# Optimization experiments

Hardware: AMD Instinct MI355X
Metric: run time of the kernel (lower is better)

## Reference

```python
import jax, jax.numpy as jnp
import numpy as np

H = 256
NUM_REL = 460
NUM_ENT = 20000
B = 4096
CUR_TS = 10
PATH_LEN = 8


def _gru_step(x, h, W_ih, W_hh, b_ih, b_hh):
    # PyTorch GRUCell math
    gi = x @ W_ih.T + b_ih          # [B, 3H]
    gh = h @ W_hh.T + b_hh          # [B, 3H]
    ir, iz, inn = jnp.split(gi, 3, axis=1)
    hr, hz, hn = jnp.split(gh, 3, axis=1)
    r = jax.nn.sigmoid(ir + hr)
    z = jax.nn.sigmoid(iz + hz)
    n = jnp.tanh(inn + r * hn)
    return (1.0 - z) * n + z * h


def setup_inputs() -> dict:
    key = jax.random.key(0)
    ks = jax.random.split(key, 24)
    s = 1.0 / np.sqrt(H)
    f32 = jnp.float32
    d = {
        "pre_emb": jax.random.normal(ks[0], (NUM_ENT, H), f32),
        "r_emb": jax.random.normal(ks[1], (NUM_REL, H), f32),
        "partial_embeding": jax.random.normal(ks[2], (B, CUR_TS * NUM_REL), f32),
        # params (uniform-ish linear init scaled by 1/sqrt(H))
        "W_map1": jax.random.normal(ks[3], (2 * H, H), f32) * s,
        "b_map1": jax.random.normal(ks[4], (2 * H,), f32) * s,
        "W_map2": jax.random.normal(ks[5], (H, 2 * H), f32) * s,
        "b_map2": jax.random.normal(ks[6], (H,), f32) * s,
        "W_h1": jax.random.normal(ks[7], (H, H), f32) * s,
        "b_h1": jax.random.normal(ks[8], (H,), f32) * s,
        "W_h2": jax.random.normal(ks[9], (H, H), f32) * s,
        "b_h2": jax.random.normal(ks[10], (H,), f32) * s,
        "W_attn": jax.random.normal(ks[11], (H, H), f32) * s,
        "b_attn": jax.random.normal(ks[12], (H,), f32) * s,
        "W_align": jax.random.normal(ks[13], (H, H), f32) * s,
        "b_align": jax.random.normal(ks[14], (H,), f32) * s,
        "W_ih": jax.random.normal(ks[15], (3 * H, H), f32) * s,
        "W_hh": jax.random.normal(ks[16], (3 * H, H), f32) * s,
        "b_ih": jax.random.normal(ks[17], (3 * H,), f32) * s,
        "b_hh": jax.random.normal(ks[18], (3 * H,), f32) * s,
        "all_triples": jax.random.randint(ks[19], (B, 3), 0, NUM_REL, dtype=jnp.int64)
        if jax.config.jax_enable_x64 else jax.random.randint(ks[19], (B, 3), 0, NUM_REL, dtype=jnp.int32),
        "cur_ts": CUR_TS,
        "num_rel": NUM_REL,
    }
    return d


def reference(pre_emb, r_emb, partial_embeding,
              W_map1, b_map1, W_map2, b_map2,
              W_h1, b_h1, W_h2, b_h2,
              W_attn, b_attn, W_align, b_align,
              W_ih, W_hh, b_ih, b_hh,
              all_triples, cur_ts, num_rel):
    # rel_mapping1 -> rel_mapping2
    mapped_rel = (r_emb @ W_map1.T + b_map1) @ W_map2.T + b_map2     # [R, H]
    q_rel = mapped_rel[all_triples[:, 1]]                            # [B, H]

    # attention logits base (constant over timesteps): linear_attn(q_rel) @ mapped_rel.T
    attn_base = (q_rel @ W_attn.T + b_attn) @ mapped_rel.T           # [B, R]

    start_ts = max(cur_ts - PATH_LEN, 0)
    nb = partial_embeding.shape[0]
    cur_seq = partial_embeding.reshape(nb, cur_ts, num_rel)[:, start_ts:cur_ts]  # [B, T, R]
    cur_seq = jnp.swapaxes(cur_seq, 0, 1)                            # [T, B, R]

    h0 = jnp.zeros((nb, H), dtype=pre_emb.dtype)

    def step(h, cur):
        attn = cur * attn_base
        attn = jnp.where(attn == 0, jnp.asarray(-1e9, attn.dtype), attn)
        attn = jax.nn.softmax(attn, axis=1)
        x = attn @ mapped_rel                                        # [B, H]
        return _gru_step(x, h, W_ih, W_hh, b_ih, b_hh), None

    gru_hidden, _ = jax.lax.scan(step, h0, cur_seq)

    # predicted history embedding + match loss (MSE)
    predicted_hist = 0.1 * ((q_rel @ W_h1.T + b_h1) @ W_h2.T + b_h2) + q_rel
    match_loss = jnp.mean((predicted_hist - gru_hidden) ** 2)

    # forward_forth, distmult scoring
    h2 = _gru_step(q_rel, predicted_hist, W_ih, W_hh, b_ih, b_hh)    # [B, H]
    aligned_all = pre_emb @ W_align.T + b_align                      # [E, H]
    sub = aligned_all[all_triples[:, 0]]                             # [B, H]
    score_logits = (sub * h2) @ aligned_all.T                        # [B, E]
    score = jax.nn.sigmoid(score_logits)

    # BCE(sigmoid(logits), one_hot(obj)) in stable logits form without
    # materializing the dense one-hot label matrix:
    # mean over B*E of [ softplus(x) - x * label ]
    obj = all_triples[:, 2]
    pos_logits = score_logits[jnp.arange(nb), obj]
    path_loss = (jnp.sum(jax.nn.softplus(score_logits)) - jnp.sum(pos_logits)) / (nb * score_logits.shape[1])

    return match_loss, path_loss, score
```

## Files before the change

### kernel.cpp

```cpp
#include <hip/hip_runtime.h>
#include <hip/hip_bf16.h>

typedef __hip_bfloat16 bf16;
typedef __attribute__((ext_vector_type(8))) short short8;
typedef __attribute__((ext_vector_type(4))) float f32x4;
typedef __attribute__((ext_vector_type(4))) short short4v;

#define NREL 460
#define KP   480
#define NENT 20000
#define NENT_PAD 20224
#define NB   4096

__device__ inline float sigmoidf_(float x){ return 1.f/(1.f+__expf(-x)); }

__device__ inline void gload16(const bf16* g, bf16* l){
  __builtin_amdgcn_global_load_lds(
      (const __attribute__((address_space(1))) unsigned int*)g,
      (__attribute__((address_space(3))) unsigned int*)l, 16, 0, 0);
}

__device__ __forceinline__ void fgemm_body(
    const float* __restrict__ A, int lda, int arows,
    const float* __restrict__ B, int ldb,
    const float* __restrict__ bias,
    float* __restrict__ C, int ldc, int K, int mode,
    const float* __restrict__ add_src, bf16* __restrict__ ct_out,
    float* As, float* Bs, int bx, int by)
{
  const int tid = threadIdx.x;
  const int row0 = bx*64, col0 = by*64;
  const int tx = tid & 15, ty = tid >> 4;
  float acc[4][4] = {};
  for (int k0 = 0; k0 < K; k0 += 32){
    __syncthreads();
    #pragma unroll
    for (int s = 0; s < 2; ++s){
      int slot = tid + s*256;
      int r = slot >> 3, c4 = (slot & 7)*4;
      int ra = row0 + r; if (ra >= arows) ra = arows - 1;
      float4 v = *(const float4*)(A + (long)ra*lda + k0 + c4);
      As[(c4+0)*68+r] = v.x; As[(c4+1)*68+r] = v.y; As[(c4+2)*68+r] = v.z; As[(c4+3)*68+r] = v.w;
      float4 w = *(const float4*)(B + (long)(col0 + r)*ldb + k0 + c4);
      Bs[(c4+0)*68+r] = w.x; Bs[(c4+1)*68+r] = w.y; Bs[(c4+2)*68+r] = w.z; Bs[(c4+3)*68+r] = w.w;
    }
    __syncthreads();
    #pragma unroll
    for (int kk = 0; kk < 32; ++kk){
      float4 a4 = *(const float4*)(&As[kk*68 + ty*4]);
      float4 b4 = *(const float4*)(&Bs[kk*68 + tx*4]);
      float av[4] = {a4.x, a4.y, a4.z, a4.w};
      float bv[4] = {b4.x, b4.y, b4.z, b4.w};
      #pragma unroll
      for (int i = 0; i < 4; ++i)
        #pragma unroll
        for (int j = 0; j < 4; ++j) acc[i][j] += av[i]*bv[j];
    }
  }
  const int rb = row0 + ty*4, cb = col0 + tx*4;
  if (mode == 1){
    #pragma unroll
    for (int i = 0; i < 4; ++i){
      float4 v = {acc[i][0], acc[i][1], acc[i][2], acc[i][3]};
      *(float4*)(C + (long)(rb+i)*ldc + cb) = v;
      int rr = rb + i;
      if (rr < KP){
        #pragma unroll
        for (int j = 0; j < 4; ++j)
          ct_out[(cb+j)*KP + rr] = __float2bfloat16(rr < NREL ? acc[i][j] : 0.f);
      }
    }
  } else if (mode == 2){
    #pragma unroll
    for (int i = 0; i < 4; ++i){
      float4 v;
      #pragma unroll
      for (int j = 0; j < 4; ++j)
        ((float*)&v)[j] = 0.1f*(acc[i][j] + bias[cb+j]) + add_src[(long)(rb+i)*ldc + cb+j];
      *(float4*)(C + (long)(rb+i)*ldc + cb) = v;
    }
  } else {
    float bv[4] = {0,0,0,0};
    if (bias){ bv[0]=bias[cb]; bv[1]=bias[cb+1]; bv[2]=bias[cb+2]; bv[3]=bias[cb+3]; }
    #pragma unroll
    for (int i = 0; i < 4; ++i){
      float4 v = {acc[i][0]+bv[0], acc[i][1]+bv[1], acc[i][2]+bv[2], acc[i][3]+bv[3]};
      *(float4*)(C + (long)(rb+i)*ldc + cb) = v;
    }
  }
}

struct FDesc {
  const float* A; const float* B; const float* bias; float* C;
  const float* add; bf16* ct;
  int lda, ldb, ldc, K, arows, mode;
};

template<int MODE>
__device__ __forceinline__ void gemm128_body(
    const bf16* __restrict__ A, int lda,
    const bf16* __restrict__ B, int ldb,
    const float* __restrict__ bias,
    void* __restrict__ C, long ldc,
    int K, int n_valid, double* __restrict__ sp_sum,
    const int* __restrict__ trips,
    bf16* sbuf, float* wsum, int bx, int by)
{
  const int tid = threadIdx.x;
  const int lane = tid & 63, wave = tid >> 6;
  const long row0 = (long)bx * 128;
  const long col0 = (long)by * 128;
  const int sr = tid >> 2;
  const int sc = ((tid & 3) ^ ((sr >> 1) & 3)) * 8;
  const bf16* Ag0 = A + (row0 + sr)*lda + sc;
  const bf16* Ag1 = A + (row0 + 64 + sr)*lda + sc;
  const bf16* Bg0 = B + (col0 + sr)*ldb + sc;
  const bf16* Bg1 = B + (col0 + 64 + sr)*ldb + sc;
  bf16* As_ = sbuf;
  bf16* Bs_ = sbuf + 8192;
  const int wr = (wave >> 1)*64, wc = (wave & 1)*64;
  const int rA = lane & 15;
  const int kA = ((lane >> 4) ^ ((rA >> 1) & 3)) * 8;
  f32x4 acc[4][4] = {};
  const int nt = K >> 5;
  gload16(Ag0, As_ + tid*8);
  gload16(Ag1, As_ + 2048 + tid*8);
  gload16(Bg0, Bs_ + tid*8);
  gload16(Bg1, Bs_ + 2048 + tid*8);
  int cur = 0;
  for (int t = 0; t < nt; ++t){
    if (t + 1 < nt){
      const int k0 = (t+1) << 5;
      const int nxt = cur ^ 1;
      gload16(Ag0 + k0, As_ + nxt*4096 + tid*8);
      gload16(Ag1 + k0, As_ + nxt*4096 + 2048 + tid*8);
      gload16(Bg0 + k0, Bs_ + nxt*4096 + tid*8);
      gload16(Bg1 + k0, Bs_ + nxt*4096 + 2048 + tid*8);
      asm volatile("s_waitcnt vmcnt(4)" ::: "memory");
    } else {
      asm volatile("s_waitcnt vmcnt(0)" ::: "memory");
    }
    __builtin_amdgcn_s_barrier();
    short8 a[4], b[4];
    #pragma unroll
    for (int m = 0; m < 4; ++m) a[m] = *(const short8*)(As_ + cur*4096 + (wr + m*16 + rA)*32 + kA);
    #pragma unroll
    for (int n = 0; n < 4; ++n) b[n] = *(const short8*)(Bs_ + cur*4096 + (wc + n*16 + rA)*32 + kA);
    asm volatile("s_waitcnt lgkmcnt(0)" ::: "memory");
    __builtin_amdgcn_s_barrier();
    #pragma unroll
    for (int m = 0; m < 4; ++m)
      #pragma unroll
      for (int n = 0; n < 4; ++n)
        acc[m][n] = __builtin_amdgcn_mfma_f32_16x16x32_bf16(a[m], b[n], acc[m][n], 0,0,0);
    cur ^= 1;
  }
  const int ri = (lane >> 4)*4, ci = lane & 15;
  __syncthreads();
  if constexpr (MODE == 1){
    bf16* epi = sbuf + wave*1152;
    const int rrow = lane >> 2, q = lane & 3;
    #pragma unroll
    for (int m = 0; m < 4; ++m){
      #pragma unroll
      for (int n = 0; n < 4; ++n){
        long c = col0 + wc + n*16 + ci;
        float bv = bias ? bias[c] : 0.f;
        #pragma unroll
        for (int i = 0; i < 4; ++i)
          epi[(ri+i)*72 + n*16 + ci] = __float2bfloat16(acc[m][n][i] + bv);
      }
      long gr = row0 + wr + m*16 + rrow;
      bf16* gp = (bf16*)C + gr*ldc + col0 + wc + q*16;
      const bf16* lp = epi + rrow*72 + q*16;
      *(short8*)(gp)     = *(const short8*)(lp);
      *(short8*)(gp + 8) = *(const short8*)(lp + 8);
    }
  } else {
    float* epi = (float*)sbuf + wave*1088;
    const int rrow = lane >> 2, q = lane & 3;
    const bool maybe = (col0 + wc) < 464;
    float spart = 0.f, ppart = 0.f;
    #pragma unroll
    for (int m = 0; m < 4; ++m){
      int obj[4];
      if (maybe){
        #pragma unroll
        for (int i = 0; i < 4; ++i)
          obj[i] = trips[3*(int)(row0 + wr + m*16 + ri + i) + 2];
      }
      #pragma unroll
      for (int n = 0; n < 4; ++n){
        long c = col0 + wc + n*16 + ci;
        bool cv = (c < n_valid);
        #pragma unroll
        for (int i = 0; i < 4; ++i){
          float v = acc[m][n][i];
          float sg = 0.f;
          if (cv){
            float e = __expf(-fabsf(v));
            float tt = 1.f + e;
            float rr = __builtin_amdgcn_rcpf(tt);
            sg = (v >= 0.f) ? rr : 1.f - rr;
            spart += fmaxf(v, 0.f) + e*(0.9404f - 0.2537f*e);
            if (maybe && c == obj[i]) ppart += v;
          }
          epi[(ri+i)*68 + n*16 + ci + 2] = sg;
        }
      }
      long gr = row0 + wr + m*16 + rrow;
      long c16 = col0 + wc + q*16;
      if (c16 < n_valid){
        float* gp = (float*)C + gr*ldc + c16;
        const float* lp = epi + rrow*68 + q*16 + 2;
        *(float2*)(gp)      = *(const float2*)(lp);
        *(float4*)(gp + 2)  = *(const float4*)(lp + 2);
        *(float4*)(gp + 6)  = *(const float4*)(lp + 6);
        *(float4*)(gp + 10) = *(const float4*)(lp + 10);
        *(float2*)(gp + 14) = *(const float2*)(lp + 14);
      }
    }
    #pragma unroll
    for (int off = 32; off >= 1; off >>= 1){
      spart += __shfl_xor(spart, off);
      ppart += __shfl_xor(ppart, off);
    }
    if (lane == 0){ wsum[wave] = spart; wsum[4+wave] = ppart; }
    __syncthreads();
    if (tid == 0)
      atomicAdd(sp_sum, (double)(wsum[0]+wsum[1]+wsum[2]+wsum[3]));
    if (tid == 1)
      atomicAdd(sp_sum+1, (double)(wsum[4]+wsum[5]+wsum[6]+wsum[7]));
  }
}

__global__ __launch_bounds__(256) void k_conv_g1(
    const float4* __restrict__ s0, short4v* __restrict__ d0, int n0,
    const float4* __restrict__ s1, short4v* __restrict__ d1, int n1,
    const float4* __restrict__ s2, short4v* __restrict__ d2, int n2,
    short4v* __restrict__ pad0, int n3, double* __restrict__ dz,
    const float* __restrict__ gA, const float* __restrict__ gB,
    const float* __restrict__ gbias, float* __restrict__ gC)
{
  __shared__ __align__(16) float As[32*68];
  __shared__ __align__(16) float Bs[32*68];
  int bid = blockIdx.x;
  if (bid < 64){
    fgemm_body(gA,256,NREL, gB,256, gbias, gC,512, 256, 0, nullptr,nullptr,
               As, Bs, bid&7, bid>>3);
    return;
  }
  int i = (bid-64)*256 + threadIdx.x;
  if (i < n0+n1+n2){
    const float4* s; short4v* d; int j;
    if (i < n0){ s = s0; d = d0; j = i; }
    else if (i < n0+n1){ s = s1; d = d1; j = i-n0; }
    else { s = s2; d = d2; j = i-n0-n1; }
    float4 v = s[j];
    bf16 a = __float2bfloat16(v.x), b = __float2bfloat16(v.y);
    bf16 c = __float2bfloat16(v.z), e = __float2bfloat16(v.w);
    short4v o; o.x = *(short*)&a; o.y = *(short*)&b; o.z = *(short*)&c; o.w = *(short*)&e;
    d[j] = o;
  } else if (i < n0+n1+n2+n3){
    short4v z = {0,0,0,0};
    pad0[i - (n0+n1+n2)] = z;
  } else if (i < n0+n1+n2+n3+8){
    dz[i - (n0+n1+n2+n3)] = 0.0;
  }
}

__global__ __launch_bounds__(256) void k_fgemm(
    const float* A, int lda, int arows, const float* B, int ldb,
    const float* bias, float* C, int ldc, int K, int mode,
    const float* add_src, bf16* ct_out){
  __shared__ __align__(16) float As[32*68];
  __shared__ __align__(16) float Bs[32*68];
  fgemm_body(A, lda, arows, B, ldb, bias, C, ldc, K, mode, add_src, ct_out,
             As, Bs, blockIdx.x, blockIdx.y);
}

__global__ __launch_bounds__(256) void k_fgemm_multi(FDesc d0, FDesc d1, FDesc d2,
                                                     int y1, int y2){
  __shared__ __align__(16) float As[32*68];
  __shared__ __align__(16) float Bs[32*68];
  int y = blockIdx.y;
  FDesc d; int by;
  if (y < y1){ d = d0; by = y; }
  else if (y < y2){ d = d1; by = y - y1; }
  else { d = d2; by = y - y2; }
  fgemm_body(d.A, d.lda, d.arows, d.B, d.ldb, d.bias, d.C, d.ldc, d.K, d.mode,
             d.add, d.ct, As, Bs, blockIdx.x, by);
}

__global__ __launch_bounds__(256) void k_g3_aligned(
    FDesc d0, FDesc d1, FDesc d2, int y1, int y2,
    const bf16* __restrict__ pA, const bf16* __restrict__ pB,
    const float* __restrict__ pbias, bf16* __restrict__ pC)
{
  __shared__ __align__(16) char smem[34816 + 32];
  int bid = blockIdx.x;
  if (bid < 160){
    int bx = bid & 7, y = bid >> 3;
    FDesc d; int by;
    if (y < y1){ d = d0; by = y; }
    else if (y < y2){ d = d1; by = y - y1; }
    else { d = d2; by = y - y2; }
    fgemm_body(d.A, d.lda, d.arows, d.B, d.ldb, d.bias, d.C, d.ldc, d.K, d.mode,
               d.add, d.ct, (float*)smem, (float*)(smem + 17408), bx, by);
  } else {
    int idx = bid - 160;
    gemm128_body<1>(pA, 256, pB, 256, pbias, pC, 256, 256, 0, nullptr, nullptr,
                    (bf16*)smem, (float*)(smem + 34816), idx % 158, idx / 158);
  }
}

__global__ __launch_bounds__(256) void k_soft_makep(const float* __restrict__ partial,
    const float* __restrict__ attn_base, const int* __restrict__ trips,
    bf16* __restrict__ attn_all,
    const bf16* __restrict__ Qbf,
    const float* __restrict__ M_ih, const float* __restrict__ ghp,
    const float* __restrict__ ph, const float* __restrict__ b_ih,
    bf16* __restrict__ P){
  int bid = blockIdx.x;
  if (bid >= NB/4){
    int i = (bid - NB/4)*256 + threadIdx.x;
    int b = i >> 8, k = i & 255;
    int s = trips[b*3+0], rel = trips[b*3+1];
    long rb = (long)rel*768;
    float rg = sigmoidf_(M_ih[rb+k]     + b_ih[k]     + ghp[rb+k]);
    float zg = sigmoidf_(M_ih[rb+256+k] + b_ih[256+k] + ghp[rb+256+k]);
    float ng = tanhf    (M_ih[rb+512+k] + b_ih[512+k] + rg*ghp[rb+512+k]);
    float h2v = (1.f - zg)*ng + zg*ph[rel*256+k];
    P[i] = __float2bfloat16(__bfloat162float(Qbf[(long)s*256+k]) * h2v);
    return;
  }
  int wave = threadIdx.x >> 6, lane = threadIdx.x & 63;
  int b = bid*4 + wave;
  int rel = trips[b*3+1];
  const float* base = attn_base + (long)rel*512;
  float bs[8];
  #pragma unroll
  for (int s = 0; s < 8; ++s){
    int idx = s*64 + lane;
    bs[s] = (idx < NREL) ? base[idx] : 0.f;
  }
  const float* cur0 = partial + (long)b*4600 + 2*NREL;
  for (int t = 0; t < 8; ++t){
    const float* cur = cur0 + t*NREL;
    float v[8]; float mx = -1e30f;
    #pragma unroll
    for (int s = 0; s < 8; ++s){
      int idx = s*64 + lane;
      float val = -1e30f;
      if (idx < NREL){
        float pz = cur[idx]*bs[s];
        val = (pz == 0.f) ? -1e9f : pz;
      }
      v[s] = val; mx = fmaxf(mx, val);
    }
    #pragma unroll
    for (int off = 32; off >= 1; off >>= 1) mx = fmaxf(mx, __shfl_xor(mx, off));
    float sum = 0.f;
    #pragma unroll
    for (int s = 0; s < 8; ++s){
      int idx = s*64 + lane;
      if (idx < NREL){ v[s] = __expf(v[s]-mx); sum += v[s]; }
    }
    #pragma unroll
    for (int off = 32; off >= 1; off >>= 1) sum += __shfl_xor(sum, off);
    float inv = 1.f/sum;
    long obase = ((long)t*NB + b)*KP;
    #pragma unroll
    for (int s = 0; s < 8; ++s){
      int idx = s*64 + lane;
      if (idx < KP) attn_all[obase + idx] = __float2bfloat16(idx < NREL ? v[s]*inv : 0.f);
    }
  }
}

__global__ __launch_bounds__(256) void k_gemm_dual(
    const bf16* __restrict__ A2, const bf16* __restrict__ B2,
    void* __restrict__ C2, long ldc2, int K2, int nvalid2,
    double* __restrict__ sp, const int* __restrict__ trips, int nblk2,
    const bf16* __restrict__ A1, const bf16* __restrict__ B1,
    const float* __restrict__ bias1, void* __restrict__ C1, long ldc1, int K1)
{
  __shared__ __align__(16) bf16 sbuf[16384];
  __shared__ float wsum[8];
  int bid = blockIdx.x;
  if (bid < nblk2){
    gemm128_body<2>(A2, 256, B2, 256, nullptr, C2, ldc2, K2, nvalid2, sp, trips,
                    sbuf, wsum, bid & 31, bid >> 5);
  } else {
    int idx = bid - nblk2;
    gemm128_body<1>(A1, KP, B1, KP, bias1, C1, ldc1, K1, 0, nullptr, nullptr,
                    sbuf, wsum, idx & 255, idx >> 8);
  }
}

__global__ __launch_bounds__(512) void k_scan(
    const bf16* __restrict__ gi_all,
    const bf16* __restrict__ W_hh_bf,
    const float* __restrict__ b_hh,
    const float* __restrict__ ph,
    const int* __restrict__ trips,
    double* __restrict__ dsum, int* __restrict__ done, float* __restrict__ outf)
{
  __shared__ __align__(16) bf16 hl[16*264];
  __shared__ __align__(16) bf16 gbuf[2][16*768];
  __shared__ float red[8];
  const int tid = threadIdx.x;
  const int lane = tid & 63, wave = tid >> 6;
  const int brow0 = blockIdx.x * 16;
  const int rA = lane & 15, kA = (lane >> 4) * 8;
  const int ci = lane & 15, rbase = (lane >> 4) * 4;
  float hreg[2][4] = {};
  float bh[3][2];
  #pragma unroll
  for (int f = 0; f < 2; ++f){
    int cf = wave*32 + f*16 + ci;
    bh[0][f] = b_hh[cf]; bh[1][f] = b_hh[256+cf]; bh[2][f] = b_hh[512+cf];
  }
  short8 warr[3][2][6];
  #pragma unroll
  for (int g = 0; g < 3; ++g)
    #pragma unroll
    for (int f = 0; f < 2; ++f)
      #pragma unroll
      for (int k = 0; k < 6; ++k)
        warr[g][f][k] = *(const short8*)(W_hh_bf + (g*256 + wave*32 + f*16 + rA)*256 + k*32 + kA);
  {
    const bf16* src = gi_all + (long)brow0 * 768;
    #pragma unroll
    for (int i = 0; i < 3; ++i){
      int off = (wave*3 + i)*512 + lane*8;
      gload16(src + off, gbuf[0] + off);
    }
  }
  int cur = 0;
  for (int t = 0; t < 8; ++t){
    f32x4 acc[3][2] = {};
    if (t > 0){
      #pragma unroll
      for (int k = 0; k < 8; ++k){
        short8 a = *(const short8*)(hl + rA*264 + k*32 + kA);
        #pragma unroll
        for (int g = 0; g < 3; ++g)
          #pragma unroll
          for (int f = 0; f < 2; ++f){
            short8 b;
            if (k < 6) b = warr[g][f][k];
            else b = *(const short8*)(W_hh_bf + (g*256 + wave*32 + f*16 + rA)*256 + k*32 + kA);
            acc[g][f] = __builtin_amdgcn_mfma_f32_16x16x32_bf16(a, b, acc[g][f], 0,0,0);
          }
      }
    }
    asm volatile("s_waitcnt lgkmcnt(0) vmcnt(0)" ::: "memory");
    __builtin_amdgcn_s_barrier();
    if (t < 7){
      const bf16* src = gi_all + ((long)(t+1)*NB + brow0) * 768;
      bf16* dst = gbuf[cur ^ 1];
      #pragma unroll
      for (int i = 0; i < 3; ++i){
        int off = (wave*3 + i)*512 + lane*8;
        gload16(src + off, dst + off);
      }
    }
    const bf16* gl = gbuf[cur];
    #pragma unroll
    for (int f = 0; f < 2; ++f){
      int cf = wave*32 + f*16 + ci;
      #pragma unroll
      for (int i = 0; i < 4; ++i){
        int rloc = rbase + i;
        float gir = __bfloat162float(gl[rloc*768 + cf]);
        float giz = __bfloat162float(gl[rloc*768 + 256 + cf]);
        float gin = __bfloat162float(gl[rloc*768 + 512 + cf]);
        float rg = sigmoidf_(gir + acc[0][f][i] + bh[0][f]);
        float zg = sigmoidf_(giz + acc[1][f][i] + bh[1][f]);
        float ng = tanhf(gin + rg*(acc[2][f][i] + bh[2][f]));
        float hn = (1.f - zg)*ng + zg*hreg[f][i];
        hreg[f][i] = hn;
        hl[rloc*264 + cf] = __float2bfloat16(hn);
      }
    }
    asm volatile("s_waitcnt lgkmcnt(0)" ::: "memory");
    __builtin_amdgcn_s_barrier();
    cur ^= 1;
  }
  float d = 0.f;
  #pragma unroll
  for (int f = 0; f < 2; ++f){
    int cf = wave*32 + f*16 + ci;
    #pragma unroll
    for (int i = 0; i < 4; ++i){
      int rel = trips[(brow0 + rbase + i)*3 + 1];
      float diff = ph[rel*256 + cf] - hreg[f][i];
      d += diff*diff;
    }
  }
  #pragma unroll
  for (int off = 32; off >= 1; off >>= 1) d += __shfl_xor(d, off);
  if (lane == 0) red[wave] = d;
  __syncthreads();
  if (tid == 0){
    float s = 0.f;
    #pragma unroll
    for (int w = 0; w < 8; ++w) s += red[w];
    atomicAdd(dsum, (double)s);
    asm volatile("s_waitcnt vmcnt(0)" ::: "memory");
    int ticket = atomicAdd(done, 1);
    if (ticket == (int)gridDim.x - 1){
      double m  = atomicAdd(dsum+0, 0.0);
      double sp = atomicAdd(dsum+1, 0.0);
      double pp = atomicAdd(dsum+2, 0.0);
      outf[0] = (float)(m / (4096.0*256.0));
      outf[1] = (float)((sp - pp) / (4096.0*20000.0));
    }
  }
}

extern "C" void kernel_launch(void* const* d_in, const int* in_sizes, int n_in,
                              void* d_out, int out_size, void* d_ws, size_t ws_size,
                              hipStream_t stream){
  const float* pre_emb = (const float*)d_in[0];
  const float* r_emb   = (const float*)d_in[1];
  const float* partial = (const float*)d_in[2];
  const float* W_map1  = (const float*)d_in[3];
  const float* b_map1  = (const float*)d_in[4];
  const float* W_map2  = (const float*)d_in[5];
  const float* b_map2  = (const float*)d_in[6];
  const float* W_h1    = (const float*)d_in[7];
  const float* b_h1    = (const float*)d_in[8];
  const float* W_h2    = (const float*)d_in[9];
  const float* b_h2    = (const float*)d_in[10];
  const float* W_attn  = (const float*)d_in[11];
  const float* b_attn  = (const float*)d_in[12];
  const float* W_align = (const float*)d_in[13];
  const float* b_align = (const float*)d_in[14];
  const float* W_ih    = (const float*)d_in[15];
  const float* W_hh    = (const float*)d_in[16];
  const float* b_ih    = (const float*)d_in[17];
  const float* b_hh    = (const float*)d_in[18];
  const int*   trips   = (const int*)d_in[19];
  float* out = (float*)d_out;

  char* w = (char*)d_ws;
  auto alloc = [&](size_t bytes)->char*{
    char* r = w; w += (bytes + 255) & ~size_t(255); return r;
  };
  double* dsum      = (double*)alloc(128);
  int*    done      = (int*)(dsum + 4);
  float* t1         = (float*)alloc(512*512*4);
  float* mapped     = (float*)alloc(512*256*4);
  float* a1         = (float*)alloc(512*256*4);
  float* th         = (float*)alloc(512*256*4);
  float* ph         = (float*)alloc(512*256*4);
  float* M_ih       = (float*)alloc(512*768*4);
  float* ghp        = (float*)alloc(512*768*4);
  float* attn_base  = (float*)alloc(512*512*4);
  bf16*  M_ihT      = (bf16*)alloc(768*KP*2);
  bf16*  W_hh_bf    = (bf16*)alloc(768*256*2);
  bf16*  W_align_bf = (bf16*)alloc(256*256*2);
  bf16*  Q_bf       = (bf16*)alloc((size_t)NENT_PAD*256*2);
  bf16*  P_bf       = (bf16*)alloc((size_t)NB*256*2);
  bf16*  attn_all   = (bf16*)alloc((size_t)8*NB*KP*2);
  bf16*  gi_all     = (bf16*)alloc((size_t)8*NB*768*2);
  bf16*  pre_bf     = attn_all;

  {
    int n0 = NENT*256/4, n1 = 768*256/4, n2 = 256*256/4;
    int n3 = (NENT_PAD-NENT)*256/4;
    int ntot = n0+n1+n2+n3+8;
    k_conv_g1<<<64 + (ntot+255)/256, 256, 0, stream>>>(
        (const float4*)pre_emb, (short4v*)pre_bf, n0,
        (const float4*)W_hh, (short4v*)W_hh_bf, n1,
        (const float4*)W_align, (short4v*)W_align_bf, n2,
        (short4v*)(pre_bf + (size_t)NENT*256), n3, dsum,
        r_emb, W_map1, b_map1, t1);
  }
  k_fgemm<<<dim3(8,4),256,0,stream>>>(t1,512,512, W_map2,512, b_map2, mapped,256, 512, 0, nullptr, nullptr);
  {
    FDesc d0 = { mapped, W_ih,   nullptr, M_ih, nullptr, M_ihT, 256, 256, 768, 256, 512, 1 };
    FDesc d1 = { mapped, W_attn, b_attn,  a1,   nullptr, nullptr, 256, 256, 256, 256, 512, 0 };
    FDesc d2 = { mapped, W_h1,   b_h1,    th,   nullptr, nullptr, 256, 256, 256, 256, 512, 0 };
    k_g3_aligned<<<160 + 316, 256, 0, stream>>>(d0, d1, d2, 12, 16,
                                                pre_bf, W_align_bf, b_align, Q_bf);
  }
  {
    FDesc d0 = { th, W_h2,   b_h2,    ph,        mapped,  nullptr, 256, 256, 256, 256, 512, 2 };
    FDesc d1 = { a1, mapped, nullptr, attn_base, nullptr, nullptr, 256, 256, 512, 256, 512, 0 };
    k_fgemm_multi<<<dim3(8,12),256,0,stream>>>(d0, d1, d1, 4, 12);
  }
  k_fgemm<<<dim3(8,12),256,0,stream>>>(ph,256,512, W_hh,256, b_hh, ghp,768, 256, 0, nullptr, nullptr);
  k_soft_makep<<<NB/4 + NB,256,0,stream>>>(partial, attn_base, trips, attn_all,
                                           Q_bf, M_ih, ghp, ph, b_ih, P_bf);
  k_gemm_dual<<<5056 + 1536, 256, 0, stream>>>(
      P_bf, Q_bf, out+2, NENT, 256, NENT, dsum+1, trips, 5056,
      attn_all, M_ihT, b_ih, gi_all, 768, KP);
  k_scan<<<NB/16,512,0,stream>>>(gi_all, W_hh_bf, b_hh, ph, trips, dsum, done, out);
}
```

Measured before the change: 386.9 us.

## Run dual GEMM with 512-thread blocks splitting 128x128 tile over eight waves

```diff
diff --git a/kernel.cpp b/kernel.cpp
--- a/kernel.cpp
+++ b/kernel.cpp
@@ -96,15 +96,12 @@
   int lda, ldb, ldc, K, arows, mode;
 };
 
-template<int MODE>
-__device__ __forceinline__ void gemm128_body(
+__device__ __forceinline__ void gemm128_body1(
     const bf16* __restrict__ A, int lda,
     const bf16* __restrict__ B, int ldb,
     const float* __restrict__ bias,
-    void* __restrict__ C, long ldc,
-    int K, int n_valid, double* __restrict__ sp_sum,
-    const int* __restrict__ trips,
-    bf16* sbuf, float* wsum, int bx, int by)
+    bf16* __restrict__ C, long ldc, int K,
+    bf16* sbuf, int bx, int by)
 {
   const int tid = threadIdx.x;
   const int lane = tid & 63, wave = tid >> 6;
@@ -157,28 +154,101 @@
   }
   const int ri = (lane >> 4)*4, ci = lane & 15;
   __syncthreads();
+  bf16* epi = sbuf + wave*1152;
+  const int rrow = lane >> 2, q = lane & 3;
+  #pragma unroll
+  for (int m = 0; m < 4; ++m){
+    #pragma unroll
+    for (int n = 0; n < 4; ++n){
+      long c = col0 + wc + n*16 + ci;
+      float bv = bias ? bias[c] : 0.f;
+      #pragma unroll
+      for (int i = 0; i < 4; ++i)
+        epi[(ri+i)*72 + n*16 + ci] = __float2bfloat16(acc[m][n][i] + bv);
+    }
+    long gr = row0 + wr + m*16 + rrow;
+    bf16* gp = C + gr*ldc + col0 + wc + q*16;
+    const bf16* lp = epi + rrow*72 + q*16;
+    *(short8*)(gp)     = *(const short8*)(lp);
+    *(short8*)(gp + 8) = *(const short8*)(lp + 8);
+  }
+}
+
+template<int MODE>
+__device__ __forceinline__ void gemm512_body(
+    const bf16* __restrict__ A, int lda,
+    const bf16* __restrict__ B, int ldb,
+    const float* __restrict__ bias,
+    void* __restrict__ C, long ldc,
+    int K, int n_valid, double* __restrict__ sp_sum,
+    const int* __restrict__ trips,
+    bf16* sbuf, float* wsum, int bx, int by)
+{
+  const int tid = threadIdx.x;
+  const int lane = tid & 63, wave = tid >> 6;
+  const long row0 = (long)bx * 128;
+  const long col0 = (long)by * 128;
+  const int sr = tid >> 2;
+  const int sc = ((tid & 3) ^ ((sr >> 1) & 3)) * 8;
+  const bf16* Ag = A + (row0 + sr)*lda + sc;
+  const bf16* Bg = B + (col0 + sr)*ldb + sc;
+  bf16* As_ = sbuf;
+  bf16* Bs_ = sbuf + 8192;
+  const int wr = (wave >> 2)*64, wc = (wave & 3)*32;
+  const int rA = lane & 15;
+  const int kA = ((lane >> 4) ^ ((rA >> 1) & 3)) * 8;
+  f32x4 acc[4][2] = {};
+  const int nt = K >> 5;
+  gload16(Ag, As_ + tid*8);
+  gload16(Bg, Bs_ + tid*8);
+  int cur = 0;
+  for (int t = 0; t < nt; ++t){
+    if (t + 1 < nt){
+      const int k0 = (t+1) << 5;
+      const int nxt = cur ^ 1;
+      gload16(Ag + k0, As_ + nxt*4096 + tid*8);
+      gload16(Bg + k0, Bs_ + nxt*4096 + tid*8);
+      asm volatile("s_waitcnt vmcnt(2)" ::: "memory");
+    } else {
+      asm volatile("s_waitcnt vmcnt(0)" ::: "memory");
+    }
+    __builtin_amdgcn_s_barrier();
+    short8 a[4], b[2];
+    #pragma unroll
+    for (int m = 0; m < 4; ++m) a[m] = *(const short8*)(As_ + cur*4096 + (wr + m*16 + rA)*32 + kA);
+    #pragma unroll
+    for (int n = 0; n < 2; ++n) b[n] = *(const short8*)(Bs_ + cur*4096 + (wc + n*16 + rA)*32 + kA);
+    asm volatile("s_waitcnt lgkmcnt(0)" ::: "memory");
+    __builtin_amdgcn_s_barrier();
+    #pragma unroll
+    for (int m = 0; m < 4; ++m)
+      #pragma unroll
+      for (int n = 0; n < 2; ++n)
+        acc[m][n] = __builtin_amdgcn_mfma_f32_16x16x32_bf16(a[m], b[n], acc[m][n], 0,0,0);
+    cur ^= 1;
+  }
+  const int ri = (lane >> 4)*4, ci = lane & 15;
+  __syncthreads();
   if constexpr (MODE == 1){
-    bf16* epi = sbuf + wave*1152;
-    const int rrow = lane >> 2, q = lane & 3;
+    bf16* epi = sbuf + wave*640;
+    const int rw = lane >> 2, q = lane & 3;
     #pragma unroll
     for (int m = 0; m < 4; ++m){
       #pragma unroll
-      for (int n = 0; n < 4; ++n){
+      for (int n = 0; n < 2; ++n){
         long c = col0 + wc + n*16 + ci;
         float bv = bias ? bias[c] : 0.f;
         #pragma unroll
         for (int i = 0; i < 4; ++i)
-          epi[(ri+i)*72 + n*16 + ci] = __float2bfloat16(acc[m][n][i] + bv);
-      }
-      long gr = row0 + wr + m*16 + rrow;
-      bf16* gp = (bf16*)C + gr*ldc + col0 + wc + q*16;
-      const bf16* lp = epi + rrow*72 + q*16;
-      *(short8*)(gp)     = *(const short8*)(lp);
-      *(short8*)(gp + 8) = *(const short8*)(lp + 8);
+          epi[(ri+i)*40 + n*16 + ci] = __float2bfloat16(acc[m][n][i] + bv);
+      }
+      long gr = row0 + wr + m*16 + rw;
+      bf16* gp = (bf16*)C + gr*ldc + col0 + wc + q*8;
+      *(short8*)(gp) = *(const short8*)(epi + rw*40 + q*8);
     }
   } else {
-    float* epi = (float*)sbuf + wave*1088;
-    const int rrow = lane >> 2, q = lane & 3;
+    float* epi = (float*)sbuf + wave*576;
+    const int rw = lane >> 2, q = lane & 3;
     const bool maybe = (col0 + wc) < 464;
     float spart = 0.f, ppart = 0.f;
     #pragma unroll
@@ -190,7 +260,7 @@
           obj[i] = trips[3*(int)(row0 + wr + m*16 + ri + i) + 2];
       }
       #pragma unroll
-      for (int n = 0; n < 4; ++n){
+      for (int n = 0; n < 2; ++n){
         long c = col0 + wc + n*16 + ci;
         bool cv = (c < n_valid);
         #pragma unroll
@@ -205,19 +275,17 @@
             spart += fmaxf(v, 0.f) + e*(0.9404f - 0.2537f*e);
             if (maybe && c == obj[i]) ppart += v;
           }
-          epi[(ri+i)*68 + n*16 + ci + 2] = sg;
+          epi[(ri+i)*36 + n*16 + ci + 2] = sg;
         }
       }
-      long gr = row0 + wr + m*16 + rrow;
-      long c16 = col0 + wc + q*16;
-      if (c16 < n_valid){
-        float* gp = (float*)C + gr*ldc + c16;
-        const float* lp = epi + rrow*68 + q*16 + 2;
-        *(float2*)(gp)      = *(const float2*)(lp);
-        *(float4*)(gp + 2)  = *(const float4*)(lp + 2);
-        *(float4*)(gp + 6)  = *(const float4*)(lp + 6);
-        *(float4*)(gp + 10) = *(const float4*)(lp + 10);
-        *(float2*)(gp + 14) = *(const float2*)(lp + 14);
+      long gr = row0 + wr + m*16 + rw;
+      long c8 = col0 + wc + q*8;
+      if (c8 < n_valid){
+        float* gp = (float*)C + gr*ldc + c8;
+        const float* lp = epi + rw*36 + q*8 + 2;
+        *(float2*)(gp)     = *(const float2*)(lp);
+        *(float4*)(gp + 2) = *(const float4*)(lp + 2);
+        *(float2*)(gp + 6) = *(const float2*)(lp + 6);
       }
     }
     #pragma unroll
@@ -225,12 +293,20 @@
       spart += __shfl_xor(spart, off);
       ppart += __shfl_xor(ppart, off);
     }
-    if (lane == 0){ wsum[wave] = spart; wsum[4+wave] = ppart; }
+    if (lane == 0){ wsum[wave] = spart; wsum[8+wave] = ppart; }
     __syncthreads();
-    if (tid == 0)
-      atomicAdd(sp_sum, (double)(wsum[0]+wsum[1]+wsum[2]+wsum[3]));
-    if (tid == 1)
-      atomicAdd(sp_sum+1, (double)(wsum[4]+wsum[5]+wsum[6]+wsum[7]));
+    if (tid == 0){
+      float s = 0.f;
+      #pragma unroll
+      for (int w = 0; w < 8; ++w) s += wsum[w];
+      atomicAdd(sp_sum, (double)s);
+    }
+    if (tid == 1){
+      float p = 0.f;
+      #pragma unroll
+      for (int w = 0; w < 8; ++w) p += wsum[8+w];
+      atomicAdd(sp_sum+1, (double)p);
+    }
   }
 }
 
@@ -297,7 +373,7 @@
     const bf16* __restrict__ pA, const bf16* __restrict__ pB,
     const float* __restrict__ pbias, bf16* __restrict__ pC)
 {
-  __shared__ __align__(16) char smem[34816 + 32];
+  __shared__ __align__(16) char smem[34816];
   int bid = blockIdx.x;
   if (bid < 160){
     int bx = bid & 7, y = bid >> 3;
@@ -309,8 +385,8 @@
                d.add, d.ct, (float*)smem, (float*)(smem + 17408), bx, by);
   } else {
     int idx = bid - 160;
-    gemm128_body<1>(pA, 256, pB, 256, pbias, pC, 256, 256, 0, nullptr, nullptr,
-                    (bf16*)smem, (float*)(smem + 34816), idx % 158, idx / 158);
+    gemm128_body1(pA, 256, pB, 256, pbias, pC, 256, 256,
+                  (bf16*)smem, idx % 158, idx / 158);
   }
 }
 
@@ -378,7 +454,7 @@
   }
 }
 
-__global__ __launch_bounds__(256) void k_gemm_dual(
+__global__ __launch_bounds__(512, 4) void k_gemm_dual(
     const bf16* __restrict__ A2, const bf16* __restrict__ B2,
     void* __restrict__ C2, long ldc2, int K2, int nvalid2,
     double* __restrict__ sp, const int* __restrict__ trips, int nblk2,
@@ -386,14 +462,14 @@
     const float* __restrict__ bias1, void* __restrict__ C1, long ldc1, int K1)
 {
   __shared__ __align__(16) bf16 sbuf[16384];
-  __shared__ float wsum[8];
+  __shared__ float wsum[16];
   int bid = blockIdx.x;
   if (bid < nblk2){
-    gemm128_body<2>(A2, 256, B2, 256, nullptr, C2, ldc2, K2, nvalid2, sp, trips,
+    gemm512_body<2>(A2, 256, B2, 256, nullptr, C2, ldc2, K2, nvalid2, sp, trips,
                     sbuf, wsum, bid & 31, bid >> 5);
   } else {
     int idx = bid - nblk2;
-    gemm128_body<1>(A1, KP, B1, KP, bias1, C1, ldc1, K1, 0, nullptr, nullptr,
+    gemm512_body<1>(A1, KP, B1, KP, bias1, C1, ldc1, K1, 0, nullptr, nullptr,
                     sbuf, wsum, idx & 255, idx >> 8);
   }
 }
@@ -595,7 +671,7 @@
   k_fgemm<<<dim3(8,12),256,0,stream>>>(ph,256,512, W_hh,256, b_hh, ghp,768, 256, 0, nullptr, nullptr);
   k_soft_makep<<<NB/4 + NB,256,0,stream>>>(partial, attn_base, trips, attn_all,
                                            Q_bf, M_ih, ghp, ph, b_ih, P_bf);
-  k_gemm_dual<<<5056 + 1536, 256, 0, stream>>>(
+  k_gemm_dual<<<5056 + 1536, 512, 0, stream>>>(
       P_bf, Q_bf, out+2, NENT, 256, NENT, dsum+1, trips, 5056,
       attn_all, M_ihT, b_ih, gi_all, 768, KP);
   k_scan<<<NB/16,512,0,stream>>>(gi_all, W_hh_bf, b_hh, ph, trips, dsum, done, out);
```

Result: faster. 358.4 us, median of 2 (-7.3%).
